# Kernel tuning notes

Measured on AMD Instinct MI355X. Metric: run time of the kernel, lower is better.

Reference implementation:

```python
import jax, jax.numpy as jnp
import numpy as np

B, C, H, W, NH = 8, 192, 128, 128, 6  # batch, channels, height, width, heads


def setup_inputs() -> dict:
    key = jax.random.key(0)
    ks = jax.random.split(key, 5)
    return {
        "x": jax.random.normal(ks[0], (B, C, H, W), jnp.float32),
        "w_qkv": jax.random.normal(ks[1], (3 * C, 1, 3, 3), jnp.float32) * 0.1,  # grouped conv, groups=C
        "b_qkv": jax.random.normal(ks[2], (3 * C,), jnp.float32) * 0.1,
        "temperature": jnp.ones((NH, 1, 1), jnp.float32),
        "w_out": jax.random.normal(ks[3], (C, C), jnp.float32) * 0.05,  # 1x1 conv as dense
        "b_out": jax.random.normal(ks[4], (C,), jnp.float32) * 0.05,
    }


def reference(x, w_qkv, b_qkv, temperature, w_out, b_out):
    b, c, h, w = x.shape
    nh = temperature.shape[0]
    # grouped 3x3 conv (groups = in_ch), padding=1
    qkv = jax.lax.conv_general_dilated(
        x, w_qkv, window_strides=(1, 1), padding=[(1, 1), (1, 1)],
        feature_group_count=c, dimension_numbers=("NCHW", "OIHW", "NCHW"),
    ) + b_qkv[None, :, None, None]
    q, k, v = jnp.split(qkv, 3, axis=1)  # each [b, c, h, w]

    def to_heads(t):
        return t.reshape(b, nh, c // nh, h * w)  # b head c (h w)

    q, k, v = to_heads(q), to_heads(k), to_heads(v)
    eps = 1e-12  # F.normalize default
    q = q / jnp.maximum(jnp.linalg.norm(q, axis=-1, keepdims=True), eps)
    k = k / jnp.maximum(jnp.linalg.norm(k, axis=-1, keepdims=True), eps)
    attn = jnp.einsum("bhcn,bhdn->bhcd", q, k) * temperature[None]  # [b, nh, c/nh, c/nh]
    attn = jax.nn.softmax(attn, axis=-1)
    out = jnp.einsum("bhcd,bhdn->bhcn", attn, v).reshape(b, c, h, w)
    out = jnp.einsum("oc,bchw->bohw", w_out, out) + b_out[None, :, None, None]
    return out
```

## Files before the change

### kernel.cpp

```cpp
#include <hip/hip_runtime.h>
#include <hip/hip_bf16.h>

constexpr int B   = 8;
constexpr int Cc  = 192;
constexpr int H   = 128;
constexpr int Wd  = 128;
constexpr int NH  = 6;
constexpr int HW  = H * Wd;
constexpr int QKV = 3 * Cc;

typedef short s16x8 __attribute__((ext_vector_type(8)));
typedef float f32x16 __attribute__((ext_vector_type(16)));

constexpr size_t OFF_QKV  = 0;
constexpr size_t OFF_ATTN = 150994944ULL;
constexpr size_t OFF_SSQ  = OFF_ATTN + 196608ULL;
constexpr size_t OFF_M    = OFF_SSQ + 12288ULL;
constexpr int    N_ZERO   = (196608 + 12288) / 4;

__device__ inline unsigned short f2bf(float f) {
    __hip_bfloat16 h = __float2bfloat16(f);
    return *(unsigned short*)&h;
}

__global__ void zero_kernel(float* __restrict__ p, int n) {
    int i = blockIdx.x * 256 + threadIdx.x;
    if (i < n) p[i] = 0.f;
}

constexpr int TS = 16;

__global__ __launch_bounds__(256) void conv_qkv(
    const float* __restrict__ x, const float* __restrict__ w,
    const float* __restrict__ bias, unsigned short* __restrict__ qkv,
    float* __restrict__ ssq)
{
    int tile = blockIdx.x;
    int g    = blockIdx.y;
    int b    = blockIdx.z;
    int y0   = tile * TS;

    __shared__ float sm[TS + 2][132];
    __shared__ float red[256];

    const float* xp = x + ((size_t)b * Cc + g) * HW;
    for (int i = threadIdx.x; i < (TS + 2) * 32; i += 256) {
        int r = i >> 5, c4 = (i & 31) * 4;
        int y = y0 - 1 + r;
        if (y >= 0 && y < H) {
            float4 v4 = *(const float4*)(xp + (size_t)y * Wd + c4);
            sm[r][c4 + 1] = v4.x; sm[r][c4 + 2] = v4.y;
            sm[r][c4 + 3] = v4.z; sm[r][c4 + 4] = v4.w;
        } else {
            sm[r][c4 + 1] = 0.f; sm[r][c4 + 2] = 0.f;
            sm[r][c4 + 3] = 0.f; sm[r][c4 + 4] = 0.f;
        }
    }
    for (int i = threadIdx.x; i < (TS + 2) * 2; i += 256) {
        int r = i >> 1;
        sm[r][(i & 1) ? 129 : 0] = 0.f;
    }
    __syncthreads();

    float wreg[3][9], breg[3];
    for (int j = 0; j < 3; ++j) {
        const float* wp = w + (size_t)(3 * g + j) * 9;
        for (int t = 0; t < 9; ++t) wreg[j][t] = wp[t];
        breg[j] = bias[3 * g + j];
    }

    bool track = (g < 128);
    float ss[3] = {0.f, 0.f, 0.f};

    int xq = (threadIdx.x & 31) * 4;
    int ys = threadIdx.x >> 5;

    for (int yy = ys; yy < TS; yy += 8) {
        float rv[3][6];
        for (int r = 0; r < 3; ++r) {
            float4 a4 = *(const float4*)&sm[yy + r][xq];
            float2 a2 = *(const float2*)&sm[yy + r][xq + 4];
            rv[r][0] = a4.x; rv[r][1] = a4.y; rv[r][2] = a4.z;
            rv[r][3] = a4.w; rv[r][4] = a2.x; rv[r][5] = a2.y;
        }
        for (int j = 0; j < 3; ++j) {
            unsigned short pk[4];
            for (int xx = 0; xx < 4; ++xx) {
                float s = breg[j]
                    + wreg[j][0] * rv[0][xx] + wreg[j][1] * rv[0][xx + 1] + wreg[j][2] * rv[0][xx + 2]
                    + wreg[j][3] * rv[1][xx] + wreg[j][4] * rv[1][xx + 1] + wreg[j][5] * rv[1][xx + 2]
                    + wreg[j][6] * rv[2][xx] + wreg[j][7] * rv[2][xx + 1] + wreg[j][8] * rv[2][xx + 2];
                if (track) ss[j] += s * s;
                pk[xx] = f2bf(s);
            }
            unsigned short* op = qkv + ((size_t)b * QKV + 3 * g + j) * HW
                                     + (size_t)(y0 + yy) * Wd + xq;
            *(ushort4*)op = make_ushort4(pk[0], pk[1], pk[2], pk[3]);
        }
    }

    if (track) {
        for (int j = 0; j < 3; ++j) {
            red[threadIdx.x] = ss[j];
            __syncthreads();
            for (int st = 128; st > 0; st >>= 1) {
                if (threadIdx.x < st) red[threadIdx.x] += red[threadIdx.x + st];
                __syncthreads();
            }
            if (threadIdx.x == 0) {
                int o = 3 * g + j;
                atomicAdd(&ssq[(o < Cc ? 0 : 1) * B * Cc + b * Cc + (o % Cc)], red[0]);
            }
            __syncthreads();
        }
    }
}

constexpr int NSEG = 64;
constexpr int SEGN = HW / NSEG;

__global__ __launch_bounds__(256) void qk_mfma(
    const unsigned short* __restrict__ qkv, float* __restrict__ attn)
{
    int h = blockIdx.y, b = blockIdx.z;
    int tid = threadIdx.x;
    int wv = tid >> 6, lane = tid & 63;
    int seg = blockIdx.x * 4 + wv;
    int col = lane & 31, half = lane >> 5;

    __shared__ float sacc[1024];
    for (int i = tid; i < 1024; i += 256) sacc[i] = 0.f;
    __syncthreads();

    const unsigned short* qp = qkv + ((size_t)b * QKV + h * 32 + col) * HW
                                   + seg * SEGN + half * 8;
    const unsigned short* kp = qp + (size_t)Cc * HW;

    f32x16 acc0, acc1;
    for (int i = 0; i < 16; ++i) { acc0[i] = 0.f; acc1[i] = 0.f; }

    for (int kk = 0; kk < SEGN; kk += 32) {
        s16x8 a0 = *(const s16x8*)(qp + kk);
        s16x8 b0 = *(const s16x8*)(kp + kk);
        acc0 = __builtin_amdgcn_mfma_f32_32x32x16_bf16(a0, b0, acc0, 0, 0, 0);
        s16x8 a1 = *(const s16x8*)(qp + kk + 16);
        s16x8 b1 = *(const s16x8*)(kp + kk + 16);
        acc1 = __builtin_amdgcn_mfma_f32_32x32x16_bf16(a1, b1, acc1, 0, 0, 0);
    }

    int rb = half * 4;
    for (int r = 0; r < 16; ++r) {
        int row = (r & 3) + 8 * (r >> 2) + rb;
        atomicAdd(&sacc[row * 32 + col], acc0[r] + acc1[r]);
    }
    __syncthreads();
    float* ap = attn + (size_t)(b * NH + h) * 1024;
    for (int i = tid; i < 1024; i += 256) atomicAdd(&ap[i], sacc[i]);
}

__global__ void softmax_attn(float* __restrict__ attn,
                             const float* __restrict__ ssq,
                             const float* __restrict__ temp)
{
    int h = blockIdx.x % NH, b = blockIdx.x / NH;
    __shared__ float nk[32];
    if (threadIdx.x < 32)
        nk[threadIdx.x] = fmaxf(sqrtf(ssq[B * Cc + b * Cc + h * 32 + threadIdx.x]), 1e-12f);
    __syncthreads();
    int c = threadIdx.x;
    if (c >= 32) return;
    float nq = fmaxf(sqrtf(ssq[b * Cc + h * 32 + c]), 1e-12f);
    float t = temp[h];
    float* ap = attn + ((size_t)(b * NH + h) * 32 + c) * 32;
    float row[32];
    float mx = -1e30f;
    for (int d = 0; d < 32; ++d) {
        float v = ap[d] / (nq * nk[d]) * t;
        row[d] = v;
        mx = fmaxf(mx, v);
    }
    float sum = 0.f;
    for (int d = 0; d < 32; ++d) { row[d] = expf(row[d] - mx); sum += row[d]; }
    float inv = 1.f / sum;
    for (int d = 0; d < 32; ++d) ap[d] = row[d] * inv;
}

__global__ __launch_bounds__(256) void make_m(
    const float* __restrict__ attn, const float* __restrict__ w_out,
    unsigned short* __restrict__ M)
{
    int h = blockIdx.x, b = blockIdx.y;
    __shared__ float as[32][33];
    for (int i = threadIdx.x; i < 1024; i += 256)
        as[i / 32][i % 32] = attn[(size_t)((b * NH + h) * 32 + i / 32) * 32 + i % 32];
    __syncthreads();
    for (int i = threadIdx.x; i < Cc * 32; i += 256) {
        int o = i / 32, d = i % 32;
        const float* wp = w_out + (size_t)o * Cc + h * 32;
        float s = 0.f;
        for (int cp = 0; cp < 32; ++cp) s += wp[cp] * as[cp][d];
        M[((size_t)b * Cc + o) * Cc + h * 32 + d] = f2bf(s);
    }
}

constexpr int BN = 128;

__global__ __launch_bounds__(256) void out_gemm(
    const unsigned short* __restrict__ M, const unsigned short* __restrict__ qkv,
    const float* __restrict__ b_out, float* __restrict__ out)
{
    int n0 = blockIdx.x * BN;
    int b  = blockIdx.y;

    const unsigned short* vp = qkv + ((size_t)b * QKV + 2 * Cc) * HW;
    const unsigned short* mp = M + (size_t)b * Cc * Cc;

    __shared__ unsigned short vsT[BN][24];

    int tid  = threadIdx.x;
    int lane = tid & 63, wv = tid >> 6;
    int wm = wv & 1, wn = wv >> 1;
    int col = lane & 31, half = lane >> 5;

    f32x16 acc[6];
    for (int t = 0; t < 6; ++t)
        for (int i = 0; i < 16; ++i) acc[t][i] = 0.f;

    int p  = tid >> 5;
    int nq = tid & 31;

    for (int k0 = 0; k0 < Cc; k0 += 16) {
        const unsigned short* s0 = vp + (size_t)(k0 + 2 * p) * HW + n0 + 4 * nq;
        ushort4 va = *(const ushort4*)s0;
        ushort4 vb = *(const ushort4*)(s0 + HW);
        *(unsigned int*)&vsT[4 * nq + 0][2 * p] = (unsigned int)va.x | ((unsigned int)vb.x << 16);
        *(unsigned int*)&vsT[4 * nq + 1][2 * p] = (unsigned int)va.y | ((unsigned int)vb.y << 16);
        *(unsigned int*)&vsT[4 * nq + 2][2 * p] = (unsigned int)va.z | ((unsigned int)vb.z << 16);
        *(unsigned int*)&vsT[4 * nq + 3][2 * p] = (unsigned int)va.w | ((unsigned int)vb.w << 16);
        __syncthreads();

        s16x8 af[3], bf[2];
        for (int mt = 0; mt < 3; ++mt) {
            int o = wm * 96 + mt * 32 + col;
            af[mt] = *(const s16x8*)(mp + (size_t)o * Cc + k0 + half * 8);
        }
        for (int nt = 0; nt < 2; ++nt) {
            int nn = wn * 64 + nt * 32 + col;
            bf[nt] = *(const s16x8*)&vsT[nn][half * 8];
        }
        for (int mt = 0; mt < 3; ++mt)
            for (int nt = 0; nt < 2; ++nt)
                acc[mt * 2 + nt] = __builtin_amdgcn_mfma_f32_32x32x16_bf16(
                    af[mt], bf[nt], acc[mt * 2 + nt], 0, 0, 0);
        __syncthreads();
    }

    for (int mt = 0; mt < 3; ++mt)
        for (int nt = 0; nt < 2; ++nt) {
            f32x16 c = acc[mt * 2 + nt];
            int n = n0 + wn * 64 + nt * 32 + col;
            for (int r = 0; r < 16; ++r) {
                int row = (r & 3) + 8 * (r >> 2) + 4 * half;
                int o = wm * 96 + mt * 32 + row;
                out[((size_t)b * Cc + o) * HW + n] = c[r] + b_out[o];
            }
        }
}

extern "C" void kernel_launch(void* const* d_in, const int* in_sizes, int n_in,
                              void* d_out, int out_size, void* d_ws, size_t ws_size,
                              hipStream_t stream) {
    const float* x      = (const float*)d_in[0];
    const float* w_qkv  = (const float*)d_in[1];
    const float* b_qkv  = (const float*)d_in[2];
    const float* temp   = (const float*)d_in[3];
    const float* w_out  = (const float*)d_in[4];
    const float* b_out  = (const float*)d_in[5];
    float* out = (float*)d_out;

    char* ws = (char*)d_ws;
    unsigned short* qkv = (unsigned short*)(ws + OFF_QKV);
    float* attn         = (float*)(ws + OFF_ATTN);
    float* ssq          = (float*)(ws + OFF_SSQ);
    unsigned short* M   = (unsigned short*)(ws + OFF_M);

    zero_kernel<<<(N_ZERO + 255) / 256, 256, 0, stream>>>(attn, N_ZERO);
    conv_qkv<<<dim3(H / TS, Cc, B), 256, 0, stream>>>(x, w_qkv, b_qkv, qkv, ssq);
    qk_mfma<<<dim3(NSEG / 4, NH, B), 256, 0, stream>>>(qkv, attn);
    softmax_attn<<<B * NH, 64, 0, stream>>>(attn, ssq, temp);
    make_m<<<dim3(NH, B), 256, 0, stream>>>(attn, w_out, M);
    out_gemm<<<dim3(HW / BN, B), 256, 0, stream>>>(M, qkv, b_out, out);
}
```

Measured before the change: 289.2 us.

## Remove shared-memory staging and block barriers from conv, qk reduction, and output GEMM

The depthwise conv now has each thread load its own three input rows (8 outputs per thread) from global memory, with no shared tile and no block barrier. The qk kernel writes per-wave partials to separate shared buffers instead of using shared atomics. The output GEMM gives each wave its own 32-column slice and all 192 output rows, with a wave-private transposed V tile, wave barriers only, and register prefetch of the next V chunk. The intent is to remove block-level synchronisation and atomic contention, at the cost of redundant halo loads in the conv and more per-wave reloads of M in the GEMM.

```diff
diff --git a/kernel.cpp b/kernel.cpp
--- a/kernel.cpp
+++ b/kernel.cpp
@@ -9,6 +9,7 @@
 constexpr int HW  = H * Wd;
 constexpr int QKV = 3 * Cc;
 
+typedef short s16x4 __attribute__((ext_vector_type(4)));
 typedef short s16x8 __attribute__((ext_vector_type(8)));
 typedef float f32x16 __attribute__((ext_vector_type(16)));
 
@@ -38,29 +39,28 @@
     int tile = blockIdx.x;
     int g    = blockIdx.y;
     int b    = blockIdx.z;
-    int y0   = tile * TS;
-
-    __shared__ float sm[TS + 2][132];
-    __shared__ float red[256];
+    int tid  = threadIdx.x;
+    int y    = tile * TS + (tid >> 4);
+    int xq   = (tid & 15) * 8;
 
     const float* xp = x + ((size_t)b * Cc + g) * HW;
-    for (int i = threadIdx.x; i < (TS + 2) * 32; i += 256) {
-        int r = i >> 5, c4 = (i & 31) * 4;
-        int y = y0 - 1 + r;
-        if (y >= 0 && y < H) {
-            float4 v4 = *(const float4*)(xp + (size_t)y * Wd + c4);
-            sm[r][c4 + 1] = v4.x; sm[r][c4 + 2] = v4.y;
-            sm[r][c4 + 3] = v4.z; sm[r][c4 + 4] = v4.w;
+
+    float r[3][10];
+    for (int dr = 0; dr < 3; ++dr) {
+        int yy = y - 1 + dr;
+        bool vy = (yy >= 0) && (yy < H);
+        const float* rp = xp + (size_t)yy * Wd;
+        if (vy) {
+            float4 a4 = *(const float4*)(rp + xq);
+            float4 b4 = *(const float4*)(rp + xq + 4);
+            r[dr][0] = (xq > 0)   ? rp[xq - 1] : 0.f;
+            r[dr][1] = a4.x; r[dr][2] = a4.y; r[dr][3] = a4.z; r[dr][4] = a4.w;
+            r[dr][5] = b4.x; r[dr][6] = b4.y; r[dr][7] = b4.z; r[dr][8] = b4.w;
+            r[dr][9] = (xq < 120) ? rp[xq + 8] : 0.f;
         } else {
-            sm[r][c4 + 1] = 0.f; sm[r][c4 + 2] = 0.f;
-            sm[r][c4 + 3] = 0.f; sm[r][c4 + 4] = 0.f;
-        }
-    }
-    for (int i = threadIdx.x; i < (TS + 2) * 2; i += 256) {
-        int r = i >> 1;
-        sm[r][(i & 1) ? 129 : 0] = 0.f;
-    }
-    __syncthreads();
+            for (int i = 0; i < 10; ++i) r[dr][i] = 0.f;
+        }
+    }
 
     float wreg[3][9], breg[3];
     for (int j = 0; j < 3; ++j) {
@@ -72,42 +72,37 @@
     bool track = (g < 128);
     float ss[3] = {0.f, 0.f, 0.f};
 
-    int xq = (threadIdx.x & 31) * 4;
-    int ys = threadIdx.x >> 5;
-
-    for (int yy = ys; yy < TS; yy += 8) {
-        float rv[3][6];
-        for (int r = 0; r < 3; ++r) {
-            float4 a4 = *(const float4*)&sm[yy + r][xq];
-            float2 a2 = *(const float2*)&sm[yy + r][xq + 4];
-            rv[r][0] = a4.x; rv[r][1] = a4.y; rv[r][2] = a4.z;
-            rv[r][3] = a4.w; rv[r][4] = a2.x; rv[r][5] = a2.y;
-        }
+    for (int j = 0; j < 3; ++j) {
+        unsigned short pk[8];
+        for (int xx = 0; xx < 8; ++xx) {
+            float s = breg[j];
+            for (int dr = 0; dr < 3; ++dr)
+                s += wreg[j][dr * 3 + 0] * r[dr][xx]
+                   + wreg[j][dr * 3 + 1] * r[dr][xx + 1]
+                   + wreg[j][dr * 3 + 2] * r[dr][xx + 2];
+            if (track) ss[j] += s * s;
+            pk[xx] = f2bf(s);
+        }
+        unsigned short* op = qkv + ((size_t)b * QKV + 3 * g + j) * HW
+                                 + (size_t)y * Wd + xq;
+        uint4 uu;
+        uu.x = (unsigned int)pk[0] | ((unsigned int)pk[1] << 16);
+        uu.y = (unsigned int)pk[2] | ((unsigned int)pk[3] << 16);
+        uu.z = (unsigned int)pk[4] | ((unsigned int)pk[5] << 16);
+        uu.w = (unsigned int)pk[6] | ((unsigned int)pk[7] << 16);
+        *(uint4*)op = uu;
+    }
+
+    if (track) {
+        __shared__ float red[256];
         for (int j = 0; j < 3; ++j) {
-            unsigned short pk[4];
-            for (int xx = 0; xx < 4; ++xx) {
-                float s = breg[j]
-                    + wreg[j][0] * rv[0][xx] + wreg[j][1] * rv[0][xx + 1] + wreg[j][2] * rv[0][xx + 2]
-                    + wreg[j][3] * rv[1][xx] + wreg[j][4] * rv[1][xx + 1] + wreg[j][5] * rv[1][xx + 2]
-                    + wreg[j][6] * rv[2][xx] + wreg[j][7] * rv[2][xx + 1] + wreg[j][8] * rv[2][xx + 2];
-                if (track) ss[j] += s * s;
-                pk[xx] = f2bf(s);
-            }
-            unsigned short* op = qkv + ((size_t)b * QKV + 3 * g + j) * HW
-                                     + (size_t)(y0 + yy) * Wd + xq;
-            *(ushort4*)op = make_ushort4(pk[0], pk[1], pk[2], pk[3]);
-        }
-    }
-
-    if (track) {
-        for (int j = 0; j < 3; ++j) {
-            red[threadIdx.x] = ss[j];
+            red[tid] = ss[j];
             __syncthreads();
             for (int st = 128; st > 0; st >>= 1) {
-                if (threadIdx.x < st) red[threadIdx.x] += red[threadIdx.x + st];
+                if (tid < st) red[tid] += red[tid + st];
                 __syncthreads();
             }
-            if (threadIdx.x == 0) {
+            if (tid == 0) {
                 int o = 3 * g + j;
                 atomicAdd(&ssq[(o < Cc ? 0 : 1) * B * Cc + b * Cc + (o % Cc)], red[0]);
             }
@@ -128,9 +123,7 @@
     int seg = blockIdx.x * 4 + wv;
     int col = lane & 31, half = lane >> 5;
 
-    __shared__ float sacc[1024];
-    for (int i = tid; i < 1024; i += 256) sacc[i] = 0.f;
-    __syncthreads();
+    __shared__ float sred[4][1024];
 
     const unsigned short* qp = qkv + ((size_t)b * QKV + h * 32 + col) * HW
                                    + seg * SEGN + half * 8;
@@ -151,11 +144,12 @@
     int rb = half * 4;
     for (int r = 0; r < 16; ++r) {
         int row = (r & 3) + 8 * (r >> 2) + rb;
-        atomicAdd(&sacc[row * 32 + col], acc0[r] + acc1[r]);
+        sred[wv][row * 32 + col] = acc0[r] + acc1[r];
     }
     __syncthreads();
     float* ap = attn + (size_t)(b * NH + h) * 1024;
-    for (int i = tid; i < 1024; i += 256) atomicAdd(&ap[i], sacc[i]);
+    for (int i = tid; i < 1024; i += 256)
+        atomicAdd(&ap[i], sred[0][i] + sred[1][i] + sred[2][i] + sred[3][i]);
 }
 
 __global__ void softmax_attn(float* __restrict__ attn,
@@ -209,62 +203,57 @@
     const unsigned short* __restrict__ M, const unsigned short* __restrict__ qkv,
     const float* __restrict__ b_out, float* __restrict__ out)
 {
-    int n0 = blockIdx.x * BN;
-    int b  = blockIdx.y;
-
-    const unsigned short* vp = qkv + ((size_t)b * QKV + 2 * Cc) * HW;
+    int tid  = threadIdx.x;
+    int wv   = tid >> 6, lane = tid & 63;
+    int b    = blockIdx.y;
+    int n0   = blockIdx.x * BN + wv * 32;
+    int col  = lane & 31, half = lane >> 5;
+    int a    = lane >> 3;
+    int bq   = lane & 7;
+
+    __shared__ unsigned short vsT[4][32][20];
+    unsigned short (*vt)[20] = vsT[wv];
+
+    const unsigned short* vp = qkv + ((size_t)b * QKV + 2 * Cc) * HW + n0 + 4 * bq;
     const unsigned short* mp = M + (size_t)b * Cc * Cc;
-
-    __shared__ unsigned short vsT[BN][24];
-
-    int tid  = threadIdx.x;
-    int lane = tid & 63, wv = tid >> 6;
-    int wm = wv & 1, wn = wv >> 1;
-    int col = lane & 31, half = lane >> 5;
 
     f32x16 acc[6];
     for (int t = 0; t < 6; ++t)
         for (int i = 0; i < 16; ++i) acc[t][i] = 0.f;
 
-    int p  = tid >> 5;
-    int nq = tid & 31;
+    const unsigned short* s0 = vp + (size_t)(2 * a) * HW;
+    ushort4 va = *(const ushort4*)s0;
+    ushort4 vb = *(const ushort4*)(s0 + HW);
 
     for (int k0 = 0; k0 < Cc; k0 += 16) {
-        const unsigned short* s0 = vp + (size_t)(k0 + 2 * p) * HW + n0 + 4 * nq;
-        ushort4 va = *(const ushort4*)s0;
-        ushort4 vb = *(const ushort4*)(s0 + HW);
-        *(unsigned int*)&vsT[4 * nq + 0][2 * p] = (unsigned int)va.x | ((unsigned int)vb.x << 16);
-        *(unsigned int*)&vsT[4 * nq + 1][2 * p] = (unsigned int)va.y | ((unsigned int)vb.y << 16);
-        *(unsigned int*)&vsT[4 * nq + 2][2 * p] = (unsigned int)va.z | ((unsigned int)vb.z << 16);
-        *(unsigned int*)&vsT[4 * nq + 3][2 * p] = (unsigned int)va.w | ((unsigned int)vb.w << 16);
-        __syncthreads();
-
-        s16x8 af[3], bf[2];
-        for (int mt = 0; mt < 3; ++mt) {
-            int o = wm * 96 + mt * 32 + col;
-            af[mt] = *(const s16x8*)(mp + (size_t)o * Cc + k0 + half * 8);
-        }
-        for (int nt = 0; nt < 2; ++nt) {
-            int nn = wn * 64 + nt * 32 + col;
-            bf[nt] = *(const s16x8*)&vsT[nn][half * 8];
-        }
-        for (int mt = 0; mt < 3; ++mt)
-            for (int nt = 0; nt < 2; ++nt)
-                acc[mt * 2 + nt] = __builtin_amdgcn_mfma_f32_32x32x16_bf16(
-                    af[mt], bf[nt], acc[mt * 2 + nt], 0, 0, 0);
-        __syncthreads();
-    }
-
-    for (int mt = 0; mt < 3; ++mt)
-        for (int nt = 0; nt < 2; ++nt) {
-            f32x16 c = acc[mt * 2 + nt];
-            int n = n0 + wn * 64 + nt * 32 + col;
-            for (int r = 0; r < 16; ++r) {
-                int row = (r & 3) + 8 * (r >> 2) + 4 * half;
-                int o = wm * 96 + mt * 32 + row;
-                out[((size_t)b * Cc + o) * HW + n] = c[r] + b_out[o];
-            }
-        }
+        *(unsigned int*)&vt[4 * bq + 0][2 * a] = (unsigned int)va.x | ((unsigned int)vb.x << 16);
+        *(unsigned int*)&vt[4 * bq + 1][2 * a] = (unsigned int)va.y | ((unsigned int)vb.y << 16);
+        *(unsigned int*)&vt[4 * bq + 2][2 * a] = (unsigned int)va.z | ((unsigned int)vb.z << 16);
+        *(unsigned int*)&vt[4 * bq + 3][2 * a] = (unsigned int)va.w | ((unsigned int)vb.w << 16);
+        if (k0 + 16 < Cc) {
+            const unsigned short* s1 = vp + (size_t)(k0 + 16 + 2 * a) * HW;
+            va = *(const ushort4*)s1;
+            vb = *(const ushort4*)(s1 + HW);
+        }
+        __builtin_amdgcn_wave_barrier();
+        s16x4 lo = *(const s16x4*)&vt[col][half * 8];
+        s16x4 hi = *(const s16x4*)&vt[col][half * 8 + 4];
+        s16x8 bf = __builtin_shufflevector(lo, hi, 0, 1, 2, 3, 4, 5, 6, 7);
+        for (int mt = 0; mt < 6; ++mt) {
+            s16x8 af = *(const s16x8*)(mp + (size_t)(mt * 32 + col) * Cc + k0 + half * 8);
+            acc[mt] = __builtin_amdgcn_mfma_f32_32x32x16_bf16(af, bf, acc[mt], 0, 0, 0);
+        }
+        __builtin_amdgcn_wave_barrier();
+    }
+
+    for (int mt = 0; mt < 6; ++mt) {
+        f32x16 c = acc[mt];
+        for (int rr = 0; rr < 16; ++rr) {
+            int row = (rr & 3) + 8 * (rr >> 2) + 4 * half;
+            int o = mt * 32 + row;
+            out[((size_t)b * Cc + o) * HW + n0 + col] = c[rr] + b_out[o];
+        }
+    }
 }
 
 extern "C" void kernel_launch(void* const* d_in, const int* in_sizes, int n_in,
```

Result: slower. 298.9 us (+3.3%).
